# Performance work log

Measured on AMD Instinct MI355X. Metric: run time of the kernel, lower is better.

## Reference

```python
import jax, jax.numpy as jnp
import numpy as np

B, N = 32, 8192
NUM_CLASSES = 40
SA1_DIMS = (3, 64, 64, 128)      # grouped relative xyz only (in_channels=3 -> no extra features)
SA2_DIMS = (131, 128, 128, 256)  # 128 SA1 features + 3 relative xyz
LOC_DIMS = (256, 256, 512, 1024)
GLOB_DIMS = (1024, 512, 256)


def _fps(xyz, m):
    """Farthest point sampling. xyz: [B,N,3] -> indices [B,m] (first index is point 0)."""
    b, n, _ = xyz.shape
    big = jnp.asarray(1e10, xyz.dtype)

    def step(carry, _):
        dists, last = carry                                   # [B,N], [B]
        p = jnp.take_along_axis(xyz, last[:, None, None], axis=1)  # [B,1,3]
        d = jnp.sum((xyz - p) ** 2, axis=-1)                  # [B,N]
        dists = jnp.minimum(dists, d)
        nxt = jnp.argmax(dists, axis=-1).astype(jnp.int32)
        return (dists, nxt), nxt

    init = (jnp.full((b, n), big, xyz.dtype), jnp.zeros((b,), jnp.int32))
    _, rest = jax.lax.scan(step, init, None, length=m - 1)    # [m-1,B]
    return jnp.concatenate([jnp.zeros((b, 1), jnp.int32), rest.T], axis=1)


def _ball_query(xyz, new_xyz, radius, k):
    """First-k points within radius of each centroid, padded with the first hit (CUDA ball_query semantics)."""
    d2 = jnp.sum((new_xyz[:, :, None, :] - xyz[:, None, :, :]) ** 2, axis=-1)  # [B,M,N]
    valid = d2 < radius * radius
    n = xyz.shape[1]
    ar = jnp.arange(n, dtype=jnp.int32)
    order_key = jnp.where(valid, ar, ar + n)                  # valid points sort first, in index order
    _, idx = jax.lax.top_k(-order_key, k)                     # [B,M,K] first-k valid indices
    num_valid = jnp.sum(valid, axis=-1)                       # [B,M]
    idx = jnp.where(jnp.arange(k) < num_valid[..., None], idx, idx[..., :1])
    return idx.astype(jnp.int32)


_gather = jax.vmap(lambda p, i: p[i])  # p:[N,C], i:[M,K] -> [M,K,C], vmapped over batch


def _sa(xyz, feats, m, radius, k, ws, bs):
    """PointNetSAModule: FPS -> ball query -> group (relative xyz [+feat]) -> SharedMLP -> max over K."""
    cidx = _fps(xyz, m)
    new_xyz = jnp.take_along_axis(xyz, cidx[:, :, None], axis=1)   # [B,m,3]
    idx = _ball_query(xyz, new_xyz, radius, k)                     # [B,m,k]
    x = _gather(xyz, idx) - new_xyz[:, :, None, :]                 # [B,m,k,3]
    if feats is not None:
        x = jnp.concatenate([x, _gather(feats, idx)], axis=-1)
    for w, b in zip(ws, bs):  # Conv2d(1x1)+BN(eval, folded)+ReLU
        x = jax.nn.relu(jnp.einsum('bmkc,oc->bmko', x, w) + b)
    return new_xyz, jnp.max(x, axis=2)                             # [B,m,C_out]


def _forward(points, sa1_w0, sa1_b0, sa1_w1, sa1_b1, sa1_w2, sa1_b2,
             sa2_w0, sa2_b0, sa2_w1, sa2_b1, sa2_w2, sa2_b2,
             loc_w0, loc_b0, loc_w1, loc_b1, loc_w2, loc_b2,
             glob_w0, glob_b0, glob_w1, glob_b1, cls_w, cls_b):
    xyz = jnp.transpose(points, (0, 2, 1))                         # [B,N,3]
    new_xyz, feats = _sa(xyz, None, 512, 0.2, 32,
                         (sa1_w0, sa1_w1, sa1_w2), (sa1_b0, sa1_b1, sa1_b2))
    _, feats = _sa(new_xyz, feats, 128, 0.4, 64,
                   (sa2_w0, sa2_w1, sa2_w2), (sa2_b0, sa2_b1, sa2_b2))
    x = feats                                                      # [B,128,256]
    for w, b in ((loc_w0, loc_b0), (loc_w1, loc_b1), (loc_w2, loc_b2)):
        x = jax.nn.relu(jnp.einsum('bnc,oc->bno', x, w) + b)       # SharedMLP (Conv1d+BN+ReLU)
    x = jnp.max(x, axis=1)                                         # global max-pool -> [B,1024]
    for w, b in ((glob_w0, glob_b0), (glob_w1, glob_b1)):          # MLP (dropout in eval = identity)
        x = jax.nn.relu(x @ w.T + b)
    return x @ cls_w.T + cls_b                                     # cls_logits [B,40]


def setup_inputs() -> dict:
    key = jax.random.key(0)
    ks = iter(jax.random.split(key, 64))
    inp = {}
    # unit-cube point cloud so radii 0.2/0.4 are geometrically meaningful
    inp['points'] = jax.random.uniform(next(ks), (B, 3, N), jnp.float32, -1.0, 1.0)

    def lin(co, ci):
        return jax.random.normal(next(ks), (co, ci), jnp.float32) / np.sqrt(ci)

    for name, dims in (('sa1', SA1_DIMS), ('sa2', SA2_DIMS), ('loc', LOC_DIMS)):
        for i in range(len(dims) - 1):
            inp[f'{name}_w{i}'] = lin(dims[i + 1], dims[i])
            inp[f'{name}_b{i}'] = 0.01 * jax.random.normal(next(ks), (dims[i + 1],), jnp.float32)
    for i in range(2):
        inp[f'glob_w{i}'] = lin(GLOB_DIMS[i + 1], GLOB_DIMS[i])
        inp[f'glob_b{i}'] = 0.01 * jax.random.normal(next(ks), (GLOB_DIMS[i + 1],), jnp.float32)
    inp['cls_w'] = lin(NUM_CLASSES, GLOB_DIMS[-1])
    inp['cls_b'] = jnp.zeros((NUM_CLASSES,), jnp.float32)
    return inp


def reference(points, sa1_w0, sa1_b0, sa1_w1, sa1_b1, sa1_w2, sa1_b2,
              sa2_w0, sa2_b0, sa2_w1, sa2_b1, sa2_w2, sa2_b2,
              loc_w0, loc_b0, loc_w1, loc_b1, loc_w2, loc_b2,
              glob_w0, glob_b0, glob_w1, glob_b1, cls_w, cls_b):
    return _forward(points, sa1_w0, sa1_b0, sa1_w1, sa1_b1, sa1_w2, sa1_b2,
                    sa2_w0, sa2_b0, sa2_w1, sa2_b1, sa2_w2, sa2_b2,
                    loc_w0, loc_b0, loc_w1, loc_b1, loc_w2, loc_b2,
                    glob_w0, glob_b0, glob_w1, glob_b1, cls_w, cls_b)
```

## Files before the change

### kernel.cpp

```cpp
#include <hip/hip_runtime.h>
#include <hip/hip_bf16.h>
#include <cstdint>

#define CDIV(a,b) (((a)+(b)-1)/(b))

typedef short s8v __attribute__((ext_vector_type(8)));
typedef float f4v __attribute__((ext_vector_type(4)));
typedef float f2v __attribute__((ext_vector_type(2)));

__device__ __forceinline__ unsigned short f2bf_bits(float v) {
  __hip_bfloat16 b = __float2bfloat16(v);
  unsigned short u; __builtin_memcpy(&u, &b, 2);
  return u;
}
__device__ __forceinline__ void bsplit(float v, unsigned short& h, unsigned short& l) {
  __hip_bfloat16 hb = __float2bfloat16(v);
  float hf = __bfloat162float(hb);
  unsigned short hu; __builtin_memcpy(&hu, &hb, 2);
  h = hu;
  l = f2bf_bits(v - hf);
}

__device__ __forceinline__ void gl2lds16(const void* g, void* l, int lane) {
#if __has_builtin(__builtin_amdgcn_global_load_lds)
  __builtin_amdgcn_global_load_lds(
      (const __attribute__((address_space(1))) unsigned int*)g,
      (__attribute__((address_space(3))) unsigned int*)l, 16, 0, 0);
#else
  ((uint4*)l)[lane] = *(const uint4*)g;
#endif
}

__device__ __forceinline__ void agpr_put(float& slot, float v) {
  asm volatile("v_accvgpr_write_b32 %0, %1" : "=a"(slot) : "v"(v));
}
__device__ __forceinline__ float agpr_get(const float& slot) {
  float v;
  asm volatile("v_accvgpr_read_b32 %0, %1" : "=v"(v) : "a"(slot));
  return v;
}

__device__ __forceinline__ f2v pk_add(f2v a, f2v b) {
  f2v d; asm("v_pk_add_f32 %0, %1, %2" : "=v"(d) : "v"(a), "v"(b)); return d;
}
__device__ __forceinline__ f2v pk_mul(f2v a, f2v b) {
  f2v d; asm("v_pk_mul_f32 %0, %1, %2" : "=v"(d) : "v"(a), "v"(b)); return d;
}
__device__ __forceinline__ f2v pk_fma(f2v a, f2v b, f2v c) {
  f2v d; asm("v_pk_fma_f32 %0, %1, %2, %3" : "=v"(d) : "v"(a), "v"(b), "v"(c)); return d;
}

template<int C>
__device__ __forceinline__ unsigned dpp32(unsigned v) {
  return (unsigned)__builtin_amdgcn_update_dpp((int)v, (int)v, C, 0xF, 0xF, false);
}
template<int C>
__device__ __forceinline__ unsigned long long red_key(unsigned long long pk) {
  unsigned lo = dpp32<C>((unsigned)pk);
  unsigned hi = dpp32<C>((unsigned)(pk >> 32));
  unsigned long long p2 = ((unsigned long long)hi << 32) | lo;
  return (p2 > pk) ? p2 : pk;
}

template<int NPTS, int MOUT, int NTHR>
__global__ __launch_bounds__(NTHR, 1) void fps_kernel(
    const float* __restrict__ pts, int bstride, int cstride,
    float* __restrict__ aos, float* __restrict__ soa)
{
  constexpr int PPT = NPTS / NTHR;
  constexpr int NP2 = PPT / 2;
  constexpr int NW  = NTHR / 64;
  const int b = blockIdx.x, t = threadIdx.x;
  const int lane = t & 63;
  const int wid = t >> 6;
  const float* px = pts + (size_t)b * bstride;
  const float* py = px + cstride;
  const float* pz = px + 2 * cstride;
  __shared__ float s_x[NPTS], s_y[NPTS], s_z[NPTS];
  __shared__ unsigned long long s_key[2][NW > 1 ? NW : 1];
  __shared__ int s_out[MOUT];

  float ax[PPT], ay[PPT], az[PPT];
  f2v dsv[NP2];
#pragma unroll
  for (int j = 0; j < PPT; ++j) {
    int i = t + j * NTHR;
    float x = px[i], y = py[i], z = pz[i];
    s_x[i] = x; s_y[i] = y; s_z[i] = z;
    agpr_put(ax[j], x); agpr_put(ay[j], y); agpr_put(az[j], z);
  }
#pragma unroll
  for (int q = 0; q < NP2; ++q) dsv[q] = (f2v){1e10f, 1e10f};
  if (t == 0) s_out[0] = 0;
  float lx = px[0], ly = py[0], lz = pz[0];
  __syncthreads();

  for (int it = 1; it < MOUT; ++it) {
    const f2v nlx = (f2v){-lx, -lx};
    const f2v nly = (f2v){-ly, -ly};
    const f2v nlz = (f2v){-lz, -lz};
    float bestv = -1.0f; int bestj = 0;
#pragma unroll
    for (int q = 0; q < NP2; ++q) {
      f2v x2, y2, z2;
      x2.x = agpr_get(ax[2 * q]); x2.y = agpr_get(ax[2 * q + 1]);
      y2.x = agpr_get(ay[2 * q]); y2.y = agpr_get(ay[2 * q + 1]);
      z2.x = agpr_get(az[2 * q]); z2.y = agpr_get(az[2 * q + 1]);
      f2v dx = pk_add(x2, nlx);
      f2v dy = pk_add(y2, nly);
      f2v dz = pk_add(z2, nlz);
      f2v d2 = pk_fma(dz, dz, pk_fma(dy, dy, pk_mul(dx, dx)));
      float nd0 = fminf(dsv[q].x, d2.x);
      float nd1 = fminf(dsv[q].y, d2.y);
      dsv[q].x = nd0; dsv[q].y = nd1;
      if (nd0 > bestv) { bestv = nd0; bestj = 2 * q; }
      if (nd1 > bestv) { bestv = nd1; bestj = 2 * q + 1; }
    }
    const int besti = t + bestj * NTHR;
    unsigned long long pk =
        ((unsigned long long)__float_as_uint(bestv) << 32) | (unsigned)(~(unsigned)besti);
    pk = red_key<0x111>(pk);
    pk = red_key<0x112>(pk);
    pk = red_key<0x114>(pk);
    pk = red_key<0x118>(pk);
    pk = red_key<0x142>(pk);
    pk = red_key<0x143>(pk);
    int widx;
    if constexpr (NW == 1) {
      widx = (int)(~(unsigned)__builtin_amdgcn_readlane((int)(unsigned)pk, 63));
    } else {
      const int pb = it & 1;
      if (lane == 63) s_key[pb][wid] = pk;
      __syncthreads();
      unsigned long long ck = s_key[pb][lane & (NW - 1)];
      if (NW >= 2)  ck = red_key<0x111>(ck);
      if (NW >= 4)  ck = red_key<0x112>(ck);
      if (NW >= 8)  ck = red_key<0x114>(ck);
      if (NW >= 16) ck = red_key<0x118>(ck);
      widx = (int)(~(unsigned)__builtin_amdgcn_readlane((int)(unsigned)ck, NW - 1));
    }
    lx = s_x[widx]; ly = s_y[widx]; lz = s_z[widx];
    if (t == 0) s_out[it] = widx;
  }
  __syncthreads();
  for (int i = t; i < MOUT; i += NTHR) {
    const int idx = s_out[i];
    const float x = s_x[idx], y = s_y[idx], z = s_z[idx];
    float* a = aos + ((size_t)b * MOUT + i) * 3;
    a[0] = x; a[1] = y; a[2] = z;
    soa[(size_t)b * 3 * MOUT + i]            = x;
    soa[(size_t)b * 3 * MOUT + MOUT + i]     = y;
    soa[(size_t)b * 3 * MOUT + 2 * MOUT + i] = z;
  }
}

template<int NPTS, int KNB, int MC>
__global__ __launch_bounds__(64) void ballq_wave(
    const float* __restrict__ pts, int bstride, int cstride,
    const float* __restrict__ cents, int* __restrict__ out, float r2)
{
  constexpr int NCH = NPTS / 64;
  const int g = blockIdx.x;
  const int b = g / MC;
  const int lane = threadIdx.x;
  const float* px = pts + (size_t)b * bstride;
  const float* py = px + cstride;
  const float* pz = px + 2 * cstride;
  const float cx = cents[g * 3 + 0], cy = cents[g * 3 + 1], cz = cents[g * 3 + 2];
  __shared__ int s_idx[KNB];
  float nx = px[lane], ny = py[lane], nz = pz[lane];
  int base = 0;
  for (int c = 0; c < NCH; ++c) {
    float X = nx, Y = ny, Z = nz;
    if (c + 1 < NCH) {
      int i2 = (c + 1) * 64 + lane;
      nx = px[i2]; ny = py[i2]; nz = pz[i2];
    }
    float dx = X - cx, dy = Y - cy, dz = Z - cz;
    bool valid = (dx * dx + dy * dy + dz * dz) < r2;
    unsigned long long mask = __ballot(valid);
    int rank = __popcll(mask & ((1ull << lane) - 1ull));
    int pos = base + rank;
    if (valid && pos < KNB) s_idx[pos] = c * 64 + lane;
    base += __popcll(mask);
    if (base >= KNB) break;
  }
  int total = base < KNB ? base : KNB;
  int first = s_idx[0];
  if (lane < KNB)
    out[(size_t)g * KNB + lane] = (lane < total) ? s_idx[lane] : first;
}

__global__ __launch_bounds__(256, 1) void sa1_fused(
    const float* __restrict__ pts, const int* __restrict__ idx1,
    const float* __restrict__ cents,
    const float* __restrict__ w0, const float* __restrict__ b0,
    const unsigned short* __restrict__ w1h, const unsigned short* __restrict__ w1l,
    const float* __restrict__ b1,
    const unsigned short* __restrict__ w2h, const unsigned short* __restrict__ w2l,
    const float* __restrict__ b2,
    unsigned short* __restrict__ f1h, unsigned short* __restrict__ f1l)
{
  __shared__ __align__(16) unsigned short sY[2][128 * 72];
  __shared__ __align__(16) unsigned short sZ[2][128 * 72];
  __shared__ __align__(16) unsigned short sW[2][64 * 72];
  __shared__ float sw0[192];
  __shared__ float sb0[64];

  const int tid = threadIdx.x, lane = tid & 63, wid = tid >> 6;
  const int wm = wid & 1, wn = wid >> 1;
  const int mn15 = lane & 15, kgrp = lane >> 4;
  const int bk = blockIdx.x;

  if (tid < 192) sw0[tid] = w0[tid];
  else sb0[tid - 192] = b0[tid - 192];
  for (int gi = tid; gi < 1024; gi += 256) {
    const int pl = gi >> 9, idx = gi & 511;
    const int n = idx >> 3, k8 = idx & 7;
    const uint4 v = ((const uint4*)(pl ? w1l : w1h))[idx];
    *(uint4*)&sW[pl][n * 72 + k8 * 8] = v;
  }
  __syncthreads();

  {
    const int rl = tid >> 1, half = tid & 1;
    const int r = bk * 128 + rl;
    const int gl = r >> 5, j = r & 31, b = gl >> 9;
    const int i = idx1[(size_t)gl * 32 + j];
    const float* px = pts + (size_t)b * 24576;
    const float x = px[i]         - cents[gl * 3 + 0];
    const float y = px[8192 + i]  - cents[gl * 3 + 1];
    const float z = px[16384 + i] - cents[gl * 3 + 2];
    union { unsigned short us[32]; uint4 v[4]; } ph, pl4;
#pragma unroll
    for (int u = 0; u < 32; ++u) {
      const int o = half * 32 + u;
      float v = sw0[o * 3] * x + sw0[o * 3 + 1] * y + sw0[o * 3 + 2] * z + sb0[o];
      v = fmaxf(v, 0.f);
      bsplit(v, ph.us[u], pl4.us[u]);
    }
    const int base = rl * 72 + half * 32;
#pragma unroll
    for (int g = 0; g < 4; ++g) {
      *(uint4*)&sY[0][base + g * 8] = ph.v[g];
      *(uint4*)&sY[1][base + g * 8] = pl4.v[g];
    }
  }
  __syncthreads();

  {
    f4v acc[4][2];
#pragma unroll
    for (int a = 0; a < 4; ++a)
#pragma unroll
      for (int c = 0; c < 2; ++c) acc[a][c] = (f4v){0.f, 0.f, 0.f, 0.f};
#pragma unroll
    for (int kc = 0; kc < 2; ++kc) {
      const int k0 = kc * 32;
      s8v af[2][4], bf[2][2];
#pragma unroll
      for (int mt = 0; mt < 4; ++mt) {
        const int m = wm * 64 + mt * 16 + mn15;
        af[0][mt] = *(const s8v*)&sY[0][m * 72 + k0 + kgrp * 8];
        af[1][mt] = *(const s8v*)&sY[1][m * 72 + k0 + kgrp * 8];
      }
#pragma unroll
      for (int nt = 0; nt < 2; ++nt) {
        const int n = wn * 32 + nt * 16 + mn15;
        bf[0][nt] = *(const s8v*)&sW[0][n * 72 + k0 + kgrp * 8];
        bf[1][nt] = *(const s8v*)&sW[1][n * 72 + k0 + kgrp * 8];
      }
#pragma unroll
      for (int mt = 0; mt < 4; ++mt)
#pragma unroll
        for (int nt = 0; nt < 2; ++nt) {
          acc[mt][nt] = __builtin_amdgcn_mfma_f32_16x16x32_bf16(af[0][mt], bf[0][nt], acc[mt][nt], 0, 0, 0);
          acc[mt][nt] = __builtin_amdgcn_mfma_f32_16x16x32_bf16(af[0][mt], bf[1][nt], acc[mt][nt], 0, 0, 0);
          acc[mt][nt] = __builtin_amdgcn_mfma_f32_16x16x32_bf16(af[1][mt], bf[0][nt], acc[mt][nt], 0, 0, 0);
        }
    }
#pragma unroll
    for (int nt = 0; nt < 2; ++nt) {
      const int n = wn * 32 + nt * 16 + mn15;
      const float bv = b1[n];
#pragma unroll
      for (int mt = 0; mt < 4; ++mt)
#pragma unroll
        for (int r = 0; r < 4; ++r) {
          const int m = wm * 64 + mt * 16 + (lane >> 4) * 4 + r;
          float v = fmaxf(acc[mt][nt][r] + bv, 0.f);
          unsigned short h, l; bsplit(v, h, l);
          sZ[0][m * 72 + n] = h;
          sZ[1][m * 72 + n] = l;
        }
    }
  }
  __syncthreads();

  for (int gi = tid; gi < 2048; gi += 256) {
    const int pl = gi >> 10, idx = gi & 1023;
    const int n = idx >> 3, k8 = idx & 7;
    const uint4 v = ((const uint4*)(pl ? w2l : w2h))[idx];
    *(uint4*)&sY[pl][n * 72 + k8 * 8] = v;
  }
  __syncthreads();

  {
    f4v acc[4][4];
#pragma unroll
    for (int a = 0; a < 4; ++a)
#pragma unroll
      for (int c = 0; c < 4; ++c) acc[a][c] = (f4v){0.f, 0.f, 0.f, 0.f};
#pragma unroll
    for (int kc = 0; kc < 2; ++kc) {
      const int k0 = kc * 32;
      s8v af[2][4], bf[2][4];
#pragma unroll
      for (int mt = 0; mt < 4; ++mt) {
        const int m = wm * 64 + mt * 16 + mn15;
        af[0][mt] = *(const s8v*)&sZ[0][m * 72 + k0 + kgrp * 8];
        af[1][mt] = *(const s8v*)&sZ[1][m * 72 + k0 + kgrp * 8];
      }
#pragma unroll
      for (int nt = 0; nt < 4; ++nt) {
        const int n = wn * 64 + nt * 16 + mn15;
        bf[0][nt] = *(const s8v*)&sY[0][n * 72 + k0 + kgrp * 8];
        bf[1][nt] = *(const s8v*)&sY[1][n * 72 + k0 + kgrp * 8];
      }
#pragma unroll
      for (int mt = 0; mt < 4; ++mt)
#pragma unroll
        for (int nt = 0; nt < 4; ++nt) {
          acc[mt][nt] = __builtin_amdgcn_mfma_f32_16x16x32_bf16(af[0][mt], bf[0][nt], acc[mt][nt], 0, 0, 0);
          acc[mt][nt] = __builtin_amdgcn_mfma_f32_16x16x32_bf16(af[0][mt], bf[1][nt], acc[mt][nt], 0, 0, 0);
          acc[mt][nt] = __builtin_amdgcn_mfma_f32_16x16x32_bf16(af[1][mt], bf[0][nt], acc[mt][nt], 0, 0, 0);
        }
    }
#pragma unroll
    for (int gq = 0; gq < 2; ++gq)
#pragma unroll
      for (int nt = 0; nt < 4; ++nt) {
        const int n = wn * 64 + nt * 16 + mn15;
        float v = -1e30f;
#pragma unroll
        for (int mt = 2 * gq; mt < 2 * gq + 2; ++mt)
#pragma unroll
          for (int r = 0; r < 4; ++r) v = fmaxf(v, acc[mt][nt][r]);
        v = fmaxf(v + b2[n], 0.f);
        v = fmaxf(v, __shfl_xor(v, 16, 64));
        v = fmaxf(v, __shfl_xor(v, 32, 64));
        if (lane < 16) {
          const size_t row = (size_t)bk * 4 + wm * 2 + gq;
          unsigned short h, l; bsplit(v, h, l);
          f1h[row * 128 + n] = h;
          f1l[row * 128 + n] = l;
        }
      }
  }
}

__global__ __launch_bounds__(256, 1) void sa2_fused(
    const unsigned short* __restrict__ f1h, const unsigned short* __restrict__ f1l,
    const float* __restrict__ nx1_aos, const float* __restrict__ nx2_aos,
    const int* __restrict__ idx2,
    const unsigned short* __restrict__ w1h, const unsigned short* __restrict__ w1l,
    const float* __restrict__ b1,
    const unsigned short* __restrict__ w2h, const unsigned short* __restrict__ w2l,
    const float* __restrict__ b2,
    const unsigned short* __restrict__ w3h, const unsigned short* __restrict__ w3l,
    const float* __restrict__ b3,
    unsigned short* __restrict__ f2h, unsigned short* __restrict__ f2l)
{
  __shared__ __align__(16) unsigned short sX[2][64 * 160];
  __shared__ __align__(16) unsigned short sY[2][64 * 136];
  __shared__ __align__(16) unsigned short sW[4][2][32 * 40];

  const int tid = threadIdx.x, lane = tid & 63, wid = tid >> 6;
  const int mn15 = lane & 15, kgrp = lane >> 4;
  const int gg = blockIdx.x;
  const int bb = gg >> 7;

  {
    const int r = tid >> 2, q = tid & 3;
    const int i = idx2[(size_t)gg * 64 + r];
    const int p = bb * 512 + i;
#pragma unroll
    for (int pl = 0; pl < 2; ++pl) {
      const uint4* src = (const uint4*)((pl ? f1l : f1h) + (size_t)p * 128);
#pragma unroll
      for (int g = 0; g < 4; ++g)
        *(uint4*)&sX[pl][r * 160 + (q * 4 + g) * 8] = src[q * 4 + g];
    }
    if (q == 0) {
      union { unsigned short us[8]; uint4 v; } ph, pl4;
#pragma unroll
      for (int u = 0; u < 8; ++u) { ph.us[u] = 0; pl4.us[u] = 0; }
#pragma unroll
      for (int c = 0; c < 3; ++c) {
        float v = nx1_aos[(size_t)p * 3 + c] - nx2_aos[(size_t)gg * 3 + c];
        bsplit(v, ph.us[c], pl4.us[c]);
      }
      *(uint4*)&sX[0][r * 160 + 128] = ph.v;
      *(uint4*)&sX[1][r * 160 + 128] = pl4.v;
    } else {
      uint4 z = make_uint4(0, 0, 0, 0);
      *(uint4*)&sX[0][r * 160 + 128 + q * 8] = z;
      *(uint4*)&sX[1][r * 160 + 128 + q * 8] = z;
    }
  }
  __syncthreads();

  const int spl = lane >> 5, srow = lane & 31;
  unsigned short* swb = &sW[wid][0][0];

  {
    f4v acc[4][2];
#pragma unroll
    for (int a = 0; a < 4; ++a)
#pragma unroll
      for (int c = 0; c < 2; ++c) acc[a][c] = (f4v){0.f, 0.f, 0.f, 0.f};
    uint4 pf[4];
    {
      const unsigned short* s = (spl ? w1l : w1h) + (size_t)(wid * 32 + srow) * 160;
#pragma unroll
      for (int g = 0; g < 4; ++g) pf[g] = *(const uint4*)(s + g * 8);
    }
#pragma unroll
    for (int c = 0; c < 5; ++c) {
      unsigned short* d = swb + spl * 1280 + srow * 40;
#pragma unroll
      for (int g = 0; g < 4; ++g) *(uint4*)(d + g * 8) = pf[g];
      if (c < 4) {
        const unsigned short* s = (spl ? w1l : w1h) + (size_t)(wid * 32 + srow) * 160 + (c + 1) * 32;
#pragma unroll
        for (int g = 0; g < 4; ++g) pf[g] = *(const uint4*)(s + g * 8);
      }
      const int k0 = c * 32;
      s8v af[2][4], bf[2][2];
#pragma unroll
      for (int mt = 0; mt < 4; ++mt) {
        const int m = mt * 16 + mn15;
        af[0][mt] = *(const s8v*)&sX[0][m * 160 + k0 + kgrp * 8];
        af[1][mt] = *(const s8v*)&sX[1][m * 160 + k0 + kgrp * 8];
      }
#pragma unroll
      for (int nt = 0; nt < 2; ++nt) {
        const int nl = nt * 16 + mn15;
        bf[0][nt] = *(const s8v*)&swb[0 * 1280 + nl * 40 + kgrp * 8];
        bf[1][nt] = *(const s8v*)&swb[1 * 1280 + nl * 40 + kgrp * 8];
      }
#pragma unroll
      for (int mt = 0; mt < 4; ++mt)
#pragma unroll
        for (int nt = 0; nt < 2; ++nt) {
          acc[mt][nt] = __builtin_amdgcn_mfma_f32_16x16x32_bf16(af[0][mt], bf[0][nt], acc[mt][nt], 0, 0, 0);
          acc[mt][nt] = __builtin_amdgcn_mfma_f32_16x16x32_bf16(af[0][mt], bf[1][nt], acc[mt][nt], 0, 0, 0);
          acc[mt][nt] = __builtin_amdgcn_mfma_f32_16x16x32_bf16(af[1][mt], bf[0][nt], acc[mt][nt], 0, 0, 0);
        }
    }
#pragma unroll
    for (int nt = 0; nt < 2; ++nt) {
      const int n = wid * 32 + nt * 16 + mn15;
      const float bv = b1[n];
#pragma unroll
      for (int mt = 0; mt < 4; ++mt)
#pragma unroll
        for (int r = 0; r < 4; ++r) {
          const int m = mt * 16 + kgrp * 4 + r;
          float v = fmaxf(acc[mt][nt][r] + bv, 0.f);
          unsigned short h, l; bsplit(v, h, l);
          sY[0][m * 136 + n] = h;
          sY[1][m * 136 + n] = l;
        }
    }
  }
  __syncthreads();

  {
    f4v acc[4][2];
#pragma unroll
    for (int a = 0; a < 4; ++a)
#pragma unroll
      for (int c = 0; c < 2; ++c) acc[a][c] = (f4v){0.f, 0.f, 0.f, 0.f};
    uint4 pf[4];
    {
      const unsigned short* s = (spl ? w2l : w2h) + (size_t)(wid * 32 + srow) * 128;
#pragma unroll
      for (int g = 0; g < 4; ++g) pf[g] = *(const uint4*)(s + g * 8);
    }
#pragma unroll
    for (int c = 0; c < 4; ++c) {
      unsigned short* d = swb + spl * 1280 + srow * 40;
#pragma unroll
      for (int g = 0; g < 4; ++g) *(uint4*)(d + g * 8) = pf[g];
      if (c < 3) {
        const unsigned short* s = (spl ? w2l : w2h) + (size_t)(wid * 32 + srow) * 128 + (c + 1) * 32;
#pragma unroll
        for (int g = 0; g < 4; ++g) pf[g] = *(const uint4*)(s + g * 8);
      }
      const int k0 = c * 32;
      s8v af[2][4], bf[2][2];
#pragma unroll
      for (int mt = 0; mt < 4; ++mt) {
        const int m = mt * 16 + mn15;
        af[0][mt] = *(const s8v*)&sY[0][m * 136 + k0 + kgrp * 8];
        af[1][mt] = *(const s8v*)&sY[1][m * 136 + k0 + kgrp * 8];
      }
#pragma unroll
      for (int nt = 0; nt < 2; ++nt) {
        const int nl = nt * 16 + mn15;
        bf[0][nt] = *(const s8v*)&swb[0 * 1280 + nl * 40 + kgrp * 8];
        bf[1][nt] = *(const s8v*)&swb[1 * 1280 + nl * 40 + kgrp * 8];
      }
#pragma unroll
      for (int mt = 0; mt < 4; ++mt)
#pragma unroll
        for (int nt = 0; nt < 2; ++nt) {
          acc[mt][nt] = __builtin_amdgcn_mfma_f32_16x16x32_bf16(af[0][mt], bf[0][nt], acc[mt][nt], 0, 0, 0);
          acc[mt][nt] = __builtin_amdgcn_mfma_f32_16x16x32_bf16(af[0][mt], bf[1][nt], acc[mt][nt], 0, 0, 0);
          acc[mt][nt] = __builtin_amdgcn_mfma_f32_16x16x32_bf16(af[1][mt], bf[0][nt], acc[mt][nt], 0, 0, 0);
        }
    }
#pragma unroll
    for (int nt = 0; nt < 2; ++nt) {
      const int n = wid * 32 + nt * 16 + mn15;
      const float bv = b2[n];
#pragma unroll
      for (int mt = 0; mt < 4; ++mt)
#pragma unroll
        for (int r = 0; r < 4; ++r) {
          const int m = mt * 16 + kgrp * 4 + r;
          float v = fmaxf(acc[mt][nt][r] + bv, 0.f);
          unsigned short h, l; bsplit(v, h, l);
          sX[0][m * 136 + n] = h;
          sX[1][m * 136 + n] = l;
        }
    }
  }
  __syncthreads();

#pragma unroll
  for (int h = 0; h < 2; ++h) {
    f4v acc[4][2];
#pragma unroll
    for (int a = 0; a < 4; ++a)
#pragma unroll
      for (int c = 0; c < 2; ++c) acc[a][c] = (f4v){0.f, 0.f, 0.f, 0.f};
    const int nb = wid * 64 + h * 32;
    uint4 pf[4];
    {
      const unsigned short* s = (spl ? w3l : w3h) + (size_t)(nb + srow) * 128;
#pragma unroll
      for (int g = 0; g < 4; ++g) pf[g] = *(const uint4*)(s + g * 8);
    }
#pragma unroll
    for (int c = 0; c < 4; ++c) {
      unsigned short* d = swb + spl * 1280 + srow * 40;
#pragma unroll
      for (int g = 0; g < 4; ++g) *(uint4*)(d + g * 8) = pf[g];
      if (c < 3) {
        const unsigned short* s = (spl ? w3l : w3h) + (size_t)(nb + srow) * 128 + (c + 1) * 32;
#pragma unroll
        for (int g = 0; g < 4; ++g) pf[g] = *(const uint4*)(s + g * 8);
      }
      const int k0 = c * 32;
      s8v af[2][4], bf[2][2];
#pragma unroll
      for (int mt = 0; mt < 4; ++mt) {
        const int m = mt * 16 + mn15;
        af[0][mt] = *(const s8v*)&sX[0][m * 136 + k0 + kgrp * 8];
        af[1][mt] = *(const s8v*)&sX[1][m * 136 + k0 + kgrp * 8];
      }
#pragma unroll
      for (int nt = 0; nt < 2; ++nt) {
        const int nl = nt * 16 + mn15;
        bf[0][nt] = *(const s8v*)&swb[0 * 1280 + nl * 40 + kgrp * 8];
        bf[1][nt] = *(const s8v*)&swb[1 * 1280 + nl * 40 + kgrp * 8];
      }
#pragma unroll
      for (int mt = 0; mt < 4; ++mt)
#pragma unroll
        for (int nt = 0; nt < 2; ++nt) {
          acc[mt][nt] = __builtin_amdgcn_mfma_f32_16x16x32_bf16(af[0][mt], bf[0][nt], acc[mt][nt], 0, 0, 0);
          acc[mt][nt] = __builtin_amdgcn_mfma_f32_16x16x32_bf16(af[0][mt], bf[1][nt], acc[mt][nt], 0, 0, 0);
          acc[mt][nt] = __builtin_amdgcn_mfma_f32_16x16x32_bf16(af[1][mt], bf[0][nt], acc[mt][nt], 0, 0, 0);
        }
    }
#pragma unroll
    for (int nt = 0; nt < 2; ++nt) {
      const int n = nb + nt * 16 + mn15;
      float v = -1e30f;
#pragma unroll
      for (int mt = 0; mt < 4; ++mt)
#pragma unroll
        for (int r = 0; r < 4; ++r) v = fmaxf(v, acc[mt][nt][r]);
      v = fmaxf(v + b3[n], 0.f);
      v = fmaxf(v, __shfl_xor(v, 16, 64));
      v = fmaxf(v, __shfl_xor(v, 32, 64));
      if (lane < 16) {
        unsigned short hh, ll; bsplit(v, hh, ll);
        f2h[(size_t)gg * 256 + n] = hh;
        f2l[(size_t)gg * 256 + n] = ll;
      }
    }
  }
}

struct WSplitArgs {
  const float* src[9];
  unsigned short* h[9];
  unsigned short* l[9];
  int K[9];
  int KP[9];
  int perm[9];
  int cum[10];
};
__global__ void wsplit_all(WSplitArgs a) {
  int i = blockIdx.x * 256 + threadIdx.x;
  if (i >= a.cum[9]) return;
  int s = 0;
#pragma unroll
  for (int t = 1; t < 9; ++t) s += (i >= a.cum[t]);
  int local = i - a.cum[s];
  int KP = a.KP[s], K = a.K[s];
  int r = local / KP, k = local - r * KP;
  int oc;
  if (a.perm[s]) oc = (k < 128) ? k + 3 : (k < 131 ? k - 128 : -1);
  else           oc = (k < K) ? k : -1;
  float v = (oc >= 0) ? a.src[s][(size_t)r * K + oc] : 0.f;
  unsigned short hb, lb; bsplit(v, hb, lb);
  a.h[s][local] = hb; a.l[s][local] = lb;
}

template<int BN, int POOL>
__global__ __launch_bounds__(256, 1) void mfma_gemm(
    const unsigned short* __restrict__ Ah, const unsigned short* __restrict__ Al,
    const unsigned short* __restrict__ Wh, const unsigned short* __restrict__ Wl,
    const float* __restrict__ bias,
    unsigned short* __restrict__ Ch, unsigned short* __restrict__ Cl,
    float* __restrict__ Cf,
    unsigned short* __restrict__ Chp, unsigned short* __restrict__ Clp,
    int Kdim, int Ndim)
{
  constexpr int WTN = BN / 2, NT = WTN / 16;
  __shared__ unsigned short sA[2][128 * 32];
  __shared__ unsigned short sW[2][BN * 32];
  __shared__ float sPool[4][WTN];
  const int tid = threadIdx.x, lane = tid & 63, wid = tid >> 6;
  const int wm = wid & 1, wn = wid >> 1;
  const size_t bm0 = (size_t)blockIdx.y * 128;
  const int bn0 = blockIdx.x * BN;
  const int mn15 = lane & 15, kgrp = lane >> 4;

  f4v acc[4][NT];
#pragma unroll
  for (int a = 0; a < 4; ++a)
#pragma unroll
    for (int b = 0; b < NT; ++b) acc[a][b] = (f4v){0.f, 0.f, 0.f, 0.f};

  const int sc = lane & 3, srl = lane >> 2;

  for (int k0 = 0; k0 < Kdim; k0 += 32) {
#pragma unroll
    for (int hh = 0; hh < 2; ++hh) {
      const int R = wid * 32 + hh * 16;
      const int m = R + srl;
      const int kg = (sc - m - (m >> 2)) & 3;
      const size_t go = (bm0 + m) * (size_t)Kdim + k0 + kg * 8;
      gl2lds16(Ah + go, &sA[0][R * 32], lane);
      gl2lds16(Al + go, &sA[1][R * 32], lane);
    }
    if (BN == 128) {
#pragma unroll
      for (int hh = 0; hh < 2; ++hh) {
        const int R = wid * 32 + hh * 16;
        const int n = R + srl;
        const int kg = (sc - n - (n >> 2)) & 3;
        const size_t go = (size_t)(bn0 + n) * Kdim + k0 + kg * 8;
        gl2lds16(Wh + go, &sW[0][R * 32], lane);
        gl2lds16(Wl + go, &sW[1][R * 32], lane);
      }
    } else {
      const int R = wid * 16;
      const int n = R + srl;
      const int kg = (sc - n - (n >> 2)) & 3;
      const size_t go = (size_t)(bn0 + n) * Kdim + k0 + kg * 8;
      gl2lds16(Wh + go, &sW[0][R * 32], lane);
      gl2lds16(Wl + go, &sW[1][R * 32], lane);
    }
    __syncthreads();

    s8v af[2][4], bfr[2][NT];
#pragma unroll
    for (int mt = 0; mt < 4; ++mt) {
      const int m = wm * 64 + mt * 16 + mn15;
      const int cc = (kgrp + m + (m >> 2)) & 3;
      af[0][mt] = *(const s8v*)&sA[0][m * 32 + cc * 8];
      af[1][mt] = *(const s8v*)&sA[1][m * 32 + cc * 8];
    }
#pragma unroll
    for (int nt = 0; nt < NT; ++nt) {
      const int n = wn * WTN + nt * 16 + mn15;
      const int cc = (kgrp + n + (n >> 2)) & 3;
      bfr[0][nt] = *(const s8v*)&sW[0][n * 32 + cc * 8];
      bfr[1][nt] = *(const s8v*)&sW[1][n * 32 + cc * 8];
    }
#pragma unroll
    for (int mt = 0; mt < 4; ++mt)
#pragma unroll
      for (int nt = 0; nt < NT; ++nt) {
        acc[mt][nt] = __builtin_amdgcn_mfma_f32_16x16x32_bf16(af[0][mt], bfr[0][nt], acc[mt][nt], 0, 0, 0);
        acc[mt][nt] = __builtin_amdgcn_mfma_f32_16x16x32_bf16(af[0][mt], bfr[1][nt], acc[mt][nt], 0, 0, 0);
        acc[mt][nt] = __builtin_amdgcn_mfma_f32_16x16x32_bf16(af[1][mt], bfr[0][nt], acc[mt][nt], 0, 0, 0);
      }
    __syncthreads();
  }

  float bv[NT];
#pragma unroll
  for (int nt = 0; nt < NT; ++nt) bv[nt] = bias[bn0 + wn * WTN + nt * 16 + mn15];

  if (POOL == 0) {
#pragma unroll
    for (int mt = 0; mt < 4; ++mt)
#pragma unroll
      for (int nt = 0; nt < NT; ++nt) {
        const int n = bn0 + wn * WTN + nt * 16 + mn15;
#pragma unroll
        for (int r = 0; r < 4; ++r) {
          const size_t m = bm0 + wm * 64 + mt * 16 + (lane >> 4) * 4 + r;
          float v = fmaxf(acc[mt][nt][r] + bv[nt], 0.f);
          unsigned short h, l; bsplit(v, h, l);
          Ch[m * Ndim + n] = h;
          Cl[m * Ndim + n] = l;
        }
      }
  } else {
    float part[NT];
#pragma unroll
    for (int nt = 0; nt < NT; ++nt) {
      float v = -1e30f;
#pragma unroll
      for (int mt = 0; mt < 4; ++mt)
#pragma unroll
        for (int r = 0; r < 4; ++r) v = fmaxf(v, acc[mt][nt][r]);
      v = fmaxf(v + bv[nt], 0.f);
      v = fmaxf(v, __shfl_xor(v, 16, 64));
      v = fmaxf(v, __shfl_xor(v, 32, 64));
      part[nt] = v;
      if (lane < 16) sPool[wid][nt * 16 + mn15] = v;
    }
    __syncthreads();
    if (wm == 0 && lane < 16) {
#pragma unroll
      for (int nt = 0; nt < NT; ++nt) {
        float v = fmaxf(part[nt], sPool[wid + 1][nt * 16 + mn15]);
        const int n = bn0 + wn * WTN + nt * 16 + mn15;
        if (Cf) Cf[(size_t)(bm0 / 128) * Ndim + n] = v;
      }
    }
  }
}

__global__ __launch_bounds__(256) void head_kernel(
    const float* __restrict__ pooled,
    const float* __restrict__ w0, const float* __restrict__ b0,
    const float* __restrict__ w1, const float* __restrict__ b1,
    const float* __restrict__ wc, const float* __restrict__ bc,
    float* __restrict__ out)
{
  __shared__ float sx[1024];
  __shared__ float sy[512];
  __shared__ float sz[256];
  const int b = blockIdx.x, t = threadIdx.x;
  for (int i = t; i < 1024; i += 256) sx[i] = pooled[(size_t)b * 1024 + i];
  __syncthreads();
  for (int o = t; o < 512; o += 256) {
    const float4* w4 = (const float4*)(w0 + (size_t)o * 1024);
    const float4* x4 = (const float4*)sx;
    float acc = 0.f;
#pragma unroll 4
    for (int k = 0; k < 256; ++k) {
      float4 w = w4[k], x = x4[k];
      acc += w.x * x.x + w.y * x.y + w.z * x.z + w.w * x.w;
    }
    sy[o] = fmaxf(acc + b0[o], 0.f);
  }
  __syncthreads();
  if (t < 256) {
    const float4* w4 = (const float4*)(w1 + (size_t)t * 512);
    const float4* y4 = (const float4*)sy;
    float acc = 0.f;
#pragma unroll 4
    for (int k = 0; k < 128; ++k) {
      float4 w = w4[k], y = y4[k];
      acc += w.x * y.x + w.y * y.y + w.z * y.z + w.w * y.w;
    }
    sz[t] = fmaxf(acc + b1[t], 0.f);
  }
  __syncthreads();
  if (t < 40) {
    const float4* w4 = (const float4*)(wc + (size_t)t * 256);
    const float4* z4 = (const float4*)sz;
    float acc = 0.f;
#pragma unroll 4
    for (int k = 0; k < 64; ++k) {
      float4 w = w4[k], z = z4[k];
      acc += w.x * z.x + w.y * z.y + w.z * z.z + w.w * z.w;
    }
    out[(size_t)b * 40 + t] = acc + bc[t];
  }
}

extern "C" void kernel_launch(void* const* d_in, const int* in_sizes, int n_in,
                              void* d_out, int out_size, void* d_ws, size_t ws_size,
                              hipStream_t stream)
{
  (void)in_sizes; (void)n_in; (void)out_size; (void)ws_size;

  const float* points  = (const float*)d_in[0];
  const float* sa1_w[3] = {(const float*)d_in[1], (const float*)d_in[3], (const float*)d_in[5]};
  const float* sa1_b[3] = {(const float*)d_in[2], (const float*)d_in[4], (const float*)d_in[6]};
  const float* sa2_w[3] = {(const float*)d_in[7], (const float*)d_in[9], (const float*)d_in[11]};
  const float* sa2_b[3] = {(const float*)d_in[8], (const float*)d_in[10], (const float*)d_in[12]};
  const float* loc_w[3] = {(const float*)d_in[13], (const float*)d_in[15], (const float*)d_in[17]};
  const float* loc_b[3] = {(const float*)d_in[14], (const float*)d_in[16], (const float*)d_in[18]};
  const float* glob_w0 = (const float*)d_in[19];
  const float* glob_b0 = (const float*)d_in[20];
  const float* glob_w1 = (const float*)d_in[21];
  const float* glob_b1 = (const float*)d_in[22];
  const float* cls_w   = (const float*)d_in[23];
  const float* cls_b   = (const float*)d_in[24];

  char* base = (char*)d_ws;
  size_t off = 0;
  auto alloc = [&](size_t nbytes) -> void* {
    void* p = base + off;
    off += (nbytes + 255) & ~(size_t)255;
    return p;
  };

  const size_t XE = (size_t)4096 * 512;
  const size_t YE = (size_t)4096 * 256;
  unsigned short* Xh = (unsigned short*)alloc(XE * 2);
  unsigned short* Xl = (unsigned short*)alloc(XE * 2);
  unsigned short* Yh = (unsigned short*)alloc(YE * 2);
  unsigned short* Yl = (unsigned short*)alloc(YE * 2);
  unsigned short* f1h = (unsigned short*)alloc((size_t)16384 * 128 * 2);
  unsigned short* f1l = (unsigned short*)alloc((size_t)16384 * 128 * 2);
  unsigned short* f2h = (unsigned short*)alloc((size_t)4096 * 256 * 2);
  unsigned short* f2l = (unsigned short*)alloc((size_t)4096 * 256 * 2);

  const int  wrows[9] = {64, 64, 128, 128, 128, 256, 256, 512, 1024};
  const int  wK[9]    = {3, 64, 64, 131, 128, 128, 256, 256, 512};
  const int  wKP[9]   = {32, 64, 64, 160, 128, 128, 256, 256, 512};
  const float* wsrc[9] = {sa1_w[0], sa1_w[1], sa1_w[2],
                          sa2_w[0], sa2_w[1], sa2_w[2],
                          loc_w[0], loc_w[1], loc_w[2]};
  unsigned short *wph[9], *wpl[9];
  WSplitArgs wa;
  int cum = 0;
  for (int s = 0; s < 9; ++s) {
    size_t e = (size_t)wrows[s] * wKP[s];
    wph[s] = (unsigned short*)alloc(e * 2);
    wpl[s] = (unsigned short*)alloc(e * 2);
    wa.src[s] = wsrc[s]; wa.h[s] = wph[s]; wa.l[s] = wpl[s];
    wa.K[s] = wK[s]; wa.KP[s] = wKP[s]; wa.cum[s] = cum;
    wa.perm[s] = (s == 3) ? 1 : 0;
    cum += wrows[s] * wKP[s];
  }
  wa.cum[9] = cum;

  float* nx1_aos = (float*)alloc((size_t)32 * 512 * 3 * 4);
  float* nx1_soa = (float*)alloc((size_t)32 * 512 * 3 * 4);
  int*   idx1    = (int*)  alloc((size_t)32 * 512 * 32 * 4);
  float* nx2_aos = (float*)alloc((size_t)32 * 128 * 3 * 4);
  float* nx2_soa = (float*)alloc((size_t)32 * 128 * 3 * 4);
  int*   idx2    = (int*)  alloc((size_t)32 * 128 * 64 * 4);
  float* pooled  = (float*)alloc((size_t)32 * 1024 * 4);

  const float r2a = (float)(0.2 * 0.2);
  const float r2b = (float)(0.4 * 0.4);

  wsplit_all<<<CDIV(cum, 256), 256, 0, stream>>>(wa);

  fps_kernel<8192, 512, 1024><<<32, 1024, 0, stream>>>(points, 24576, 8192, nx1_aos, nx1_soa);
  ballq_wave<8192, 32, 512><<<32 * 512, 64, 0, stream>>>(points, 24576, 8192, nx1_aos, idx1, r2a);

  sa1_fused<<<4096, 256, 0, stream>>>(
      points, idx1, nx1_aos, sa1_w[0], sa1_b[0],
      wph[1], wpl[1], sa1_b[1], wph[2], wpl[2], sa1_b[2], f1h, f1l);

  fps_kernel<512, 128, 64><<<32, 64, 0, stream>>>(nx1_soa, 1536, 512, nx2_aos, nx2_soa);
  ballq_wave<512, 64, 128><<<32 * 128, 64, 0, stream>>>(nx1_soa, 1536, 512, nx2_aos, idx2, r2b);

  sa2_fused<<<4096, 256, 0, stream>>>(
      f1h, f1l, nx1_aos, nx2_aos, idx2,
      wph[3], wpl[3], sa2_b[0],
      wph[4], wpl[4], sa2_b[1],
      wph[5], wpl[5], sa2_b[2],
      f2h, f2l);

  mfma_gemm<128, 0><<<dim3(2, 32), 256, 0, stream>>>(
      f2h, f2l, wph[6], wpl[6], loc_b[0], Yh, Yl, nullptr, nullptr, nullptr, 256, 256);
  mfma_gemm<128, 0><<<dim3(4, 32), 256, 0, stream>>>(
      Yh, Yl, wph[7], wpl[7], loc_b[1], Xh, Xl, nullptr, nullptr, nullptr, 256, 512);
  mfma_gemm<128, 128><<<dim3(8, 32), 256, 0, stream>>>(
      Xh, Xl, wph[8], wpl[8], loc_b[2], nullptr, nullptr, pooled, nullptr, nullptr, 512, 1024);

  head_kernel<<<32, 256, 0, stream>>>(pooled, glob_w0, glob_b0,
                                      glob_w1, glob_b1, cls_w, cls_b, (float*)d_out);
}
```

Measured before the change: 1.291 ms.

## Embed second FPS into SA1 kernel blocks and widen ball-query chunking

The standalone 64-thread FPS launch for the second set-abstraction level is removed. Its work now runs in 32 extra blocks of the sa1_fused grid, as a 256-thread FPS that uses packed math and LDS key reduction, so it overlaps with SA1 MLP work. The ball query now processes 128 points per iteration with two ballots, which cuts loop overhead. The first FPS launch drops from 1024 to 512 threads, and the GEMM interface is cleaned up. The embedded FPS blocks are long serial tails that may delay kernel completion, and the FPS thread-count change could shift its latency either way.

```diff
diff --git a/kernel.cpp b/kernel.cpp
--- a/kernel.cpp
+++ b/kernel.cpp
@@ -19,16 +19,6 @@
   unsigned short hu; __builtin_memcpy(&hu, &hb, 2);
   h = hu;
   l = f2bf_bits(v - hf);
-}
-
-__device__ __forceinline__ void gl2lds16(const void* g, void* l, int lane) {
-#if __has_builtin(__builtin_amdgcn_global_load_lds)
-  __builtin_amdgcn_global_load_lds(
-      (const __attribute__((address_space(1))) unsigned int*)g,
-      (__attribute__((address_space(3))) unsigned int*)l, 16, 0, 0);
-#else
-  ((uint4*)l)[lane] = *(const uint4*)g;
-#endif
 }
 
 __device__ __forceinline__ void agpr_put(float& slot, float v) {
@@ -159,7 +149,7 @@
     const float* __restrict__ pts, int bstride, int cstride,
     const float* __restrict__ cents, int* __restrict__ out, float r2)
 {
-  constexpr int NCH = NPTS / 64;
+  constexpr int NCH = NPTS / 128;
   const int g = blockIdx.x;
   const int b = g / MC;
   const int lane = threadIdx.x;
@@ -168,27 +158,102 @@
   const float* pz = px + 2 * cstride;
   const float cx = cents[g * 3 + 0], cy = cents[g * 3 + 1], cz = cents[g * 3 + 2];
   __shared__ int s_idx[KNB];
-  float nx = px[lane], ny = py[lane], nz = pz[lane];
+  float ax0 = px[lane],      ay0 = py[lane],      az0 = pz[lane];
+  float ax1 = px[64 + lane], ay1 = py[64 + lane], az1 = pz[64 + lane];
   int base = 0;
+  const unsigned long long below = (1ull << lane) - 1ull;
   for (int c = 0; c < NCH; ++c) {
-    float X = nx, Y = ny, Z = nz;
+    float X0 = ax0, Y0 = ay0, Z0 = az0;
+    float X1 = ax1, Y1 = ay1, Z1 = az1;
     if (c + 1 < NCH) {
-      int i2 = (c + 1) * 64 + lane;
-      nx = px[i2]; ny = py[i2]; nz = pz[i2];
-    }
-    float dx = X - cx, dy = Y - cy, dz = Z - cz;
-    bool valid = (dx * dx + dy * dy + dz * dz) < r2;
-    unsigned long long mask = __ballot(valid);
-    int rank = __popcll(mask & ((1ull << lane) - 1ull));
-    int pos = base + rank;
-    if (valid && pos < KNB) s_idx[pos] = c * 64 + lane;
-    base += __popcll(mask);
+      int i0 = (c + 1) * 128 + lane;
+      ax0 = px[i0];      ay0 = py[i0];      az0 = pz[i0];
+      ax1 = px[i0 + 64]; ay1 = py[i0 + 64]; az1 = pz[i0 + 64];
+    }
+    float dx0 = X0 - cx, dy0 = Y0 - cy, dz0 = Z0 - cz;
+    float dx1 = X1 - cx, dy1 = Y1 - cy, dz1 = Z1 - cz;
+    bool v0 = (dx0 * dx0 + dy0 * dy0 + dz0 * dz0) < r2;
+    bool v1 = (dx1 * dx1 + dy1 * dy1 + dz1 * dz1) < r2;
+    unsigned long long m0 = __ballot(v0);
+    unsigned long long m1 = __ballot(v1);
+    int r0 = __popcll(m0 & below);
+    int p0 = base + r0;
+    if (v0 && p0 < KNB) s_idx[p0] = c * 128 + lane;
+    int base1 = base + __popcll(m0);
+    int r1 = __popcll(m1 & below);
+    int p1 = base1 + r1;
+    if (v1 && p1 < KNB) s_idx[p1] = c * 128 + 64 + lane;
+    base = base1 + __popcll(m1);
     if (base >= KNB) break;
   }
   int total = base < KNB ? base : KNB;
   int first = s_idx[0];
   if (lane < KNB)
     out[(size_t)g * KNB + lane] = (lane < total) ? s_idx[lane] : first;
+}
+
+__device__ void fps2_embed(
+    const float* __restrict__ soa_in, int b,
+    float* __restrict__ aos, float* __restrict__ soa,
+    float* fx, float* fy, float* fz, int* fout,
+    unsigned long long* fkey , int t)
+{
+  const int lane = t & 63, wid = t >> 6;
+  const float* px = soa_in + (size_t)b * 1536;
+  const float* py = px + 512;
+  const float* pz = px + 1024;
+  float x0, y0, z0, x1, y1, z1;
+  {
+    const int i0 = t, i1 = t + 256;
+    x0 = px[i0]; y0 = py[i0]; z0 = pz[i0];
+    x1 = px[i1]; y1 = py[i1]; z1 = pz[i1];
+    fx[i0] = x0; fy[i0] = y0; fz[i0] = z0;
+    fx[i1] = x1; fy[i1] = y1; fz[i1] = z1;
+  }
+  f2v ds = (f2v){1e10f, 1e10f};
+  if (t == 0) fout[0] = 0;
+  float lx = px[0], ly = py[0], lz = pz[0];
+  __syncthreads();
+  for (int it = 1; it < 128; ++it) {
+    f2v X = (f2v){x0, x1}, Y = (f2v){y0, y1}, Z = (f2v){z0, z1};
+    f2v dx = pk_add(X, (f2v){-lx, -lx});
+    f2v dy = pk_add(Y, (f2v){-ly, -ly});
+    f2v dz = pk_add(Z, (f2v){-lz, -lz});
+    f2v d2 = pk_fma(dz, dz, pk_fma(dy, dy, pk_mul(dx, dx)));
+    float nd0 = fminf(ds.x, d2.x);
+    float nd1 = fminf(ds.y, d2.y);
+    ds.x = nd0; ds.y = nd1;
+    float bestv = nd0; int bestj = 0;
+    if (nd1 > bestv) { bestv = nd1; bestj = 1; }
+    const int besti = t + bestj * 256;
+    unsigned long long pk =
+        ((unsigned long long)__float_as_uint(bestv) << 32) | (unsigned)(~(unsigned)besti);
+    pk = red_key<0x111>(pk);
+    pk = red_key<0x112>(pk);
+    pk = red_key<0x114>(pk);
+    pk = red_key<0x118>(pk);
+    pk = red_key<0x142>(pk);
+    pk = red_key<0x143>(pk);
+    const int pb = it & 1;
+    if (lane == 63) fkey[pb * 4 + wid] = pk;
+    __syncthreads();
+    unsigned long long ck = fkey[pb * 4 + (lane & 3)];
+    ck = red_key<0x111>(ck);
+    ck = red_key<0x112>(ck);
+    const int widx = (int)(~(unsigned)__builtin_amdgcn_readlane((int)(unsigned)ck, 3));
+    lx = fx[widx]; ly = fy[widx]; lz = fz[widx];
+    if (t == 0) fout[it] = widx;
+  }
+  __syncthreads();
+  if (t < 128) {
+    const int idx = fout[t];
+    const float x = fx[idx], y = fy[idx], z = fz[idx];
+    float* a = aos + ((size_t)b * 128 + t) * 3;
+    a[0] = x; a[1] = y; a[2] = z;
+    soa[(size_t)b * 384 + t]       = x;
+    soa[(size_t)b * 384 + 128 + t] = y;
+    soa[(size_t)b * 384 + 256 + t] = z;
+  }
 }
 
 __global__ __launch_bounds__(256, 1) void sa1_fused(
@@ -199,7 +264,9 @@
     const float* __restrict__ b1,
     const unsigned short* __restrict__ w2h, const unsigned short* __restrict__ w2l,
     const float* __restrict__ b2,
-    unsigned short* __restrict__ f1h, unsigned short* __restrict__ f1l)
+    unsigned short* __restrict__ f1h, unsigned short* __restrict__ f1l,
+    const float* __restrict__ nx1_soa, float* __restrict__ nx2_aos,
+    float* __restrict__ nx2_soa)
 {
   __shared__ __align__(16) unsigned short sY[2][128 * 72];
   __shared__ __align__(16) unsigned short sZ[2][128 * 72];
@@ -210,7 +277,17 @@
   const int tid = threadIdx.x, lane = tid & 63, wid = tid >> 6;
   const int wm = wid & 1, wn = wid >> 1;
   const int mn15 = lane & 15, kgrp = lane >> 4;
-  const int bk = blockIdx.x;
+
+  if (blockIdx.x < 32) {
+    float* fx = (float*)&sY[0][0];
+    float* fy = fx + 512;
+    float* fz = fy + 512;
+    int*   fout = (int*)(fz + 512);
+    unsigned long long* fkey = (unsigned long long*)(fout + 128);
+    fps2_embed(nx1_soa, blockIdx.x, nx2_aos, nx2_soa, fx, fy, fz, fout, fkey, tid);
+    return;
+  }
+  const int bk = blockIdx.x - 32;
 
   if (tid < 192) sw0[tid] = w0[tid];
   else sb0[tid - 192] = b0[tid - 192];
@@ -632,6 +709,16 @@
   a.h[s][local] = hb; a.l[s][local] = lb;
 }
 
+__device__ __forceinline__ void gl2lds16(const void* g, void* l, int lane) {
+#if __has_builtin(__builtin_amdgcn_global_load_lds)
+  __builtin_amdgcn_global_load_lds(
+      (const __attribute__((address_space(1))) unsigned int*)g,
+      (__attribute__((address_space(3))) unsigned int*)l, 16, 0, 0);
+#else
+  ((uint4*)l)[lane] = *(const uint4*)g;
+#endif
+}
+
 template<int BN, int POOL>
 __global__ __launch_bounds__(256, 1) void mfma_gemm(
     const unsigned short* __restrict__ Ah, const unsigned short* __restrict__ Al,
@@ -639,7 +726,6 @@
     const float* __restrict__ bias,
     unsigned short* __restrict__ Ch, unsigned short* __restrict__ Cl,
     float* __restrict__ Cf,
-    unsigned short* __restrict__ Chp, unsigned short* __restrict__ Clp,
     int Kdim, int Ndim)
 {
   constexpr int WTN = BN / 2, NT = WTN / 16;
@@ -670,18 +756,9 @@
       gl2lds16(Ah + go, &sA[0][R * 32], lane);
       gl2lds16(Al + go, &sA[1][R * 32], lane);
     }
-    if (BN == 128) {
-#pragma unroll
-      for (int hh = 0; hh < 2; ++hh) {
-        const int R = wid * 32 + hh * 16;
-        const int n = R + srl;
-        const int kg = (sc - n - (n >> 2)) & 3;
-        const size_t go = (size_t)(bn0 + n) * Kdim + k0 + kg * 8;
-        gl2lds16(Wh + go, &sW[0][R * 32], lane);
-        gl2lds16(Wl + go, &sW[1][R * 32], lane);
-      }
-    } else {
-      const int R = wid * 16;
+#pragma unroll
+    for (int hh = 0; hh < 2; ++hh) {
+      const int R = wid * 32 + hh * 16;
       const int n = R + srl;
       const int kg = (sc - n - (n >> 2)) & 3;
       const size_t go = (size_t)(bn0 + n) * Kdim + k0 + kg * 8;
@@ -884,14 +961,14 @@
 
   wsplit_all<<<CDIV(cum, 256), 256, 0, stream>>>(wa);
 
-  fps_kernel<8192, 512, 1024><<<32, 1024, 0, stream>>>(points, 24576, 8192, nx1_aos, nx1_soa);
+  fps_kernel<8192, 512, 512><<<32, 512, 0, stream>>>(points, 24576, 8192, nx1_aos, nx1_soa);
   ballq_wave<8192, 32, 512><<<32 * 512, 64, 0, stream>>>(points, 24576, 8192, nx1_aos, idx1, r2a);
 
-  sa1_fused<<<4096, 256, 0, stream>>>(
+  sa1_fused<<<32 + 4096, 256, 0, stream>>>(
       points, idx1, nx1_aos, sa1_w[0], sa1_b[0],
-      wph[1], wpl[1], sa1_b[1], wph[2], wpl[2], sa1_b[2], f1h, f1l);
-
-  fps_kernel<512, 128, 64><<<32, 64, 0, stream>>>(nx1_soa, 1536, 512, nx2_aos, nx2_soa);
+      wph[1], wpl[1], sa1_b[1], wph[2], wpl[2], sa1_b[2], f1h, f1l,
+      nx1_soa, nx2_aos, nx2_soa);
+
   ballq_wave<512, 64, 128><<<32 * 128, 64, 0, stream>>>(nx1_soa, 1536, 512, nx2_aos, idx2, r2b);
 
   sa2_fused<<<4096, 256, 0, stream>>>(
@@ -902,11 +979,11 @@
       f2h, f2l);
 
   mfma_gemm<128, 0><<<dim3(2, 32), 256, 0, stream>>>(
-      f2h, f2l, wph[6], wpl[6], loc_b[0], Yh, Yl, nullptr, nullptr, nullptr, 256, 256);
+      f2h, f2l, wph[6], wpl[6], loc_b[0], Yh, Yl, nullptr, 256, 256);
   mfma_gemm<128, 0><<<dim3(4, 32), 256, 0, stream>>>(
-      Yh, Yl, wph[7], wpl[7], loc_b[1], Xh, Xl, nullptr, nullptr, nullptr, 256, 512);
+      Yh, Yl, wph[7], wpl[7], loc_b[1], Xh, Xl, nullptr, 256, 512);
   mfma_gemm<128, 128><<<dim3(8, 32), 256, 0, stream>>>(
-      Xh, Xl, wph[8], wpl[8], loc_b[2], nullptr, nullptr, pooled, nullptr, nullptr, 512, 1024);
+      Xh, Xl, wph[8], wpl[8], loc_b[2], nullptr, nullptr, pooled, 512, 1024);
 
   head_kernel<<<32, 256, 0, stream>>>(pooled, glob_w0, glob_b0,
                                       glob_w1, glob_b1, cls_w, cls_b, (float*)d_out);
```

Result: faster. 1.157 ms (-10.4%).
